# Optimization experiments

Measured on AMD Instinct MI355X. Metric: run time of the kernel, lower is better.

## Reference

```python
import jax, jax.numpy as jnp
import numpy as np

N, D_IN, FC_DIM, GROUP, NONGT, EMB = 4096, 12544, 1024, 16, 300, 64
DG = FC_DIM // GROUP  # 64 per-head dim


def extract_position_matrix(bbox, nongt_dim):
    xmin, ymin, xmax, ymax = jnp.split(bbox, 4, axis=1)  # each [N,1]
    bw = xmax - xmin + 1.0
    bh = ymax - ymin + 1.0
    cx = 0.5 * (xmin + xmax)
    cy = 0.5 * (ymin + ymax)
    dx = jnp.log(jnp.maximum(jnp.abs((cx - cx.T) / bw), 1e-3))
    dy = jnp.log(jnp.maximum(jnp.abs((cy - cy.T) / bh), 1e-3))
    dw = jnp.log(bw / bw.T)
    dh = jnp.log(bh / bh.T)
    # slice to first nongt_dim columns, stack -> [N, nongt, 4]
    return jnp.stack([dx[:, :nongt_dim], dy[:, :nongt_dim],
                      dw[:, :nongt_dim], dh[:, :nongt_dim]], axis=2)


def extract_position_embedding(pos_mat, feat_dim=64, wave_length=1000.0):
    n8 = feat_dim // 8
    feat_range = jnp.arange(n8, dtype=pos_mat.dtype)
    dim_mat = wave_length ** (8.0 / feat_dim * feat_range)  # [8]
    div = 100.0 * pos_mat[..., None] / dim_mat              # [N,nongt,4,8]
    emb = jnp.concatenate([jnp.sin(div), jnp.cos(div)], axis=3)  # [N,nongt,4,16]
    return emb.reshape(pos_mat.shape[0], pos_mat.shape[1], feat_dim)


def attention_multi_head(feat, pos_emb, Wpos, bpos, Wq, bq, Wk, bk, Wo, bo):
    # feat: [N, 1024], pos_emb: [N, nongt, 64]
    nongt_feat = feat[:NONGT]                                   # [nongt, 1024]
    aff_w = jax.nn.relu(pos_emb @ Wpos + bpos)                  # [N, nongt, G]
    aff_w = jnp.swapaxes(aff_w, 1, 2)                           # [N, G, nongt]
    q = (feat @ Wq + bq).reshape(-1, GROUP, DG)                 # [N, G, dg]
    k = (nongt_feat @ Wk + bk).reshape(NONGT, GROUP, DG)        # [nongt, G, dg]
    aff = jnp.einsum('ngd,mgd->ngm', q, k) * (1.0 / np.sqrt(DG))  # [N, G, nongt]
    logits = jnp.log(jnp.maximum(aff_w, 1e-6)) + aff
    p = jax.nn.softmax(logits, axis=2)                          # [N, G, nongt]
    out = jnp.einsum('ngm,mc->ngc', p, nongt_feat)              # [N, G, 1024]
    # grouped 1x1 conv: group g maps 1024 -> 64 outputs
    lin = jnp.einsum('ngc,goc->ngo', out, Wo) + bo.reshape(GROUP, DG)
    return lin.reshape(feat.shape[0], FC_DIM)


def setup_inputs() -> dict:
    key = jax.random.key(0)
    ks = jax.random.split(key, 20)
    roi_feat = jax.random.normal(ks[0], (N, D_IN), dtype=jnp.float32)
    u = jax.random.uniform(ks[1], (N, 4), dtype=jnp.float32)
    x1 = u[:, 0:1] * 500.0
    y1 = u[:, 1:2] * 500.0
    bbox = jnp.concatenate([x1, y1, x1 + u[:, 2:3] * 200.0 + 1.0,
                            y1 + u[:, 3:4] * 200.0 + 1.0], axis=1)
    def lin(k, fin, fout):
        s = 1.0 / np.sqrt(fin)
        return jax.random.normal(k, (fin, fout), dtype=jnp.float32) * s
    inp = {'roi_feat': roi_feat, 'bbox': bbox,
           'W_fc1': lin(ks[2], D_IN, FC_DIM), 'b_fc1': jnp.zeros((FC_DIM,), jnp.float32),
           'W_fc2': lin(ks[3], FC_DIM, FC_DIM), 'b_fc2': jnp.zeros((FC_DIM,), jnp.float32)}
    for i, base in [(1, 4), (2, 10)]:
        inp[f'Wpos{i}'] = lin(ks[base], EMB, GROUP)
        inp[f'bpos{i}'] = jnp.zeros((GROUP,), jnp.float32)
        inp[f'Wq{i}'] = lin(ks[base + 1], FC_DIM, FC_DIM)
        inp[f'bq{i}'] = jnp.zeros((FC_DIM,), jnp.float32)
        inp[f'Wk{i}'] = lin(ks[base + 2], FC_DIM, FC_DIM)
        inp[f'bk{i}'] = jnp.zeros((FC_DIM,), jnp.float32)
        inp[f'Wo{i}'] = jax.random.normal(ks[base + 3], (GROUP, DG, FC_DIM), dtype=jnp.float32) * (1.0 / np.sqrt(FC_DIM))
        inp[f'bo{i}'] = jnp.zeros((FC_DIM,), jnp.float32)
    return inp


def reference(roi_feat, bbox, W_fc1, b_fc1, W_fc2, b_fc2,
              Wpos1, bpos1, Wq1, bq1, Wk1, bk1, Wo1, bo1,
              Wpos2, bpos2, Wq2, bq2, Wk2, bk2, Wo2, bo2):
    pos_mat = extract_position_matrix(bbox, NONGT)
    pos_emb = extract_position_embedding(pos_mat, EMB)
    x = roi_feat
    for (Wf, bf, Wp, bp, Wq, bq, Wk, bk, Wo, bo) in [
        (W_fc1, b_fc1, Wpos1, bpos1, Wq1, bq1, Wk1, bk1, Wo1, bo1),
        (W_fc2, b_fc2, Wpos2, bpos2, Wq2, bq2, Wk2, bk2, Wo2, bo2)]:
        x = x @ Wf + bf
        attn = attention_multi_head(x, pos_emb, Wp, bp, Wq, bq, Wk, bk, Wo, bo)
        x = jax.nn.relu(x + attn)
    return x
```

## Files before the change

### kernel.cpp

```cpp
#include <hip/hip_runtime.h>


using bf16x8 = __attribute__((ext_vector_type(8))) short;
using f32x4  = __attribute__((ext_vector_type(4))) float;
typedef unsigned short u16;
typedef unsigned int   u32;

#define DEV __device__ __forceinline__

DEV u32 cvtpk(float lo, float hi) {
  u32 r;
  asm("v_cvt_pk_bf16_f32 %0, %1, %2" : "=v"(r) : "v"(lo), "v"(hi));
  return r;
}
DEV u16 f2bf(float f) { return (u16)cvtpk(f, f); }
DEV float bf2f(u16 h) { return __uint_as_float(((u32)h) << 16); }

DEV f32x4 mfma16(bf16x8 a, bf16x8 b, f32x4 c) {
  return __builtin_amdgcn_mfma_f32_16x16x32_bf16(a, b, c, 0, 0, 0);
}
DEV void gload16(const u16* g, u16* l) {
  __builtin_amdgcn_global_load_lds((const __attribute__((address_space(1))) void*)g,
                                   (__attribute__((address_space(3))) void*)l, 16, 0, 0);
}

DEV void fsincos(float x, float* s, float* c) {
  float r = x * 0.15915494309189535f;
  r -= rintf(r);
  float a = r * 6.283185307179586f;
  *s = __sinf(a); *c = __cosf(a);
}

__constant__ float C100D[8] = {100.f, 42.16965034285822f, 17.78279410038923f,
                               7.498942093324559f, 3.1622776601683795f,
                               1.333521432163324f, 0.5623413251903491f,
                               0.23713737056616552f};

struct PrepPosArgs {
  const float* bbox;
  const float* Wpos1; const float* Wpos2;
  const float* bpos1; const float* bpos2;
  u16* logw1; u16* logw2;
  const float* Wo1; u16* Wo1_b;
  const float* Wo2; u16* Wo2_b;
  const float* Wfc1; u16* Wfc1_t;
  const float* wsrc[5]; u16* wdst[5];
};

__global__ __launch_bounds__(256) void prep_pos_kernel(PrepPosArgs p) {
  __shared__ u16 pool[18944];
  int b = blockIdx.x, tid = threadIdx.x;
  if (b < 4096) {
    u16* emb_s = pool;
    u16* wp_s  = pool + 5632;
    u16* lw_s  = pool + 8448;
    int n = b;
    int w = tid >> 6, l = tid & 63, h = l >> 4, l15 = l & 15;
    for (int idx = tid; idx < 1024; idx += 256) {
      int e = idx >> 4, c = idx & 15;
      wp_s[c * 88 + e]        = f2bf(p.Wpos1[idx]);
      wp_s[(16 + c) * 88 + e] = f2bf(p.Wpos2[idx]);
    }
    float4 bn = ((const float4*)p.bbox)[n];
    float bw_n = bn.z - bn.x + 1.f, bh_n = bn.w - bn.y + 1.f;
    float cx_n = 0.5f * (bn.x + bn.z), cy_n = 0.5f * (bn.y + bn.w);
    float bps0 = p.bpos1[l15], bps1 = p.bpos2[l15];
    int pr = tid >> 2, k = tid & 3;

    for (int m0 = 0; m0 < 320; m0 += 64) {
      int m = m0 + pr;
      float4 bm = ((const float4*)p.bbox)[m];
      float v;
      if (k == 0)      v = logf(fmaxf(fabsf((cx_n - 0.5f * (bm.x + bm.z)) / bw_n), 1e-3f));
      else if (k == 1) v = logf(fmaxf(fabsf((cy_n - 0.5f * (bm.y + bm.w)) / bh_n), 1e-3f));
      else if (k == 2) v = logf(bw_n / (bm.z - bm.x + 1.f));
      else             v = logf(bh_n / (bm.w - bm.y + 1.f));
      __syncthreads();
#pragma unroll
      for (int tt = 0; tt < 8; tt++) {
        float s, c; fsincos(v * C100D[tt], &s, &c);
        emb_s[pr * 88 + k * 16 + tt]     = f2bf(s);
        emb_s[pr * 88 + k * 16 + 8 + tt] = f2bf(c);
      }
      __syncthreads();
      f32x4 acc0 = {0.f, 0.f, 0.f, 0.f}, acc1 = {0.f, 0.f, 0.f, 0.f};
      bf16x8 a0 = *(const bf16x8*)&emb_s[(w * 16 + l15) * 88 + h * 8];
      bf16x8 a1 = *(const bf16x8*)&emb_s[(w * 16 + l15) * 88 + 32 + h * 8];
      bf16x8 b00 = *(const bf16x8*)&wp_s[l15 * 88 + h * 8];
      bf16x8 b01 = *(const bf16x8*)&wp_s[l15 * 88 + 32 + h * 8];
      bf16x8 b10 = *(const bf16x8*)&wp_s[(16 + l15) * 88 + h * 8];
      bf16x8 b11 = *(const bf16x8*)&wp_s[(16 + l15) * 88 + 32 + h * 8];
      acc0 = mfma16(a0, b00, acc0); acc0 = mfma16(a1, b01, acc0);
      acc1 = mfma16(a0, b10, acc1); acc1 = mfma16(a1, b11, acc1);
#pragma unroll
      for (int r = 0; r < 4; r++) {
        int mm = m0 + w * 16 + h * 4 + r;
        lw_s[l15 * 328 + mm]        = f2bf(logf(fmaxf(acc0[r] + bps0, 1e-6f)));
        lw_s[(16 + l15) * 328 + mm] = f2bf(logf(fmaxf(acc1[r] + bps1, 1e-6f)));
      }
    }
    __syncthreads();
    for (int i = tid; i < 1280; i += 256) {
      int layer = i / 640, rest = i - layer * 640;
      int gg = rest / 40, seg = rest - gg * 40;
      bf16x8 v = *(const bf16x8*)&lw_s[(layer * 16 + gg) * 328 + seg * 8];
      u16* dst = (layer ? p.logw2 : p.logw1) + ((size_t)gg * 4096 + n) * 320 + seg * 8;
      *(bf16x8*)dst = v;
    }
    return;
  }
  int b2 = b - 4096;
  if (b2 < 1024) {
    const float* src = (b2 < 512) ? p.Wo1 : p.Wo2;
    u16* dst = (b2 < 512) ? p.Wo1_b : p.Wo2_b;
    size_t i = ((size_t)(b2 & 511) * 256 + tid) * 8;
    float4 a = *(const float4*)(src + i);
    float4 c = *(const float4*)(src + i + 4);
    int4 v;
    v.x = (int)cvtpk(a.x, a.y); v.y = (int)cvtpk(a.z, a.w);
    v.z = (int)cvtpk(c.x, c.y); v.w = (int)cvtpk(c.z, c.w);
    *(int4*)(dst + i) = v;
    return;
  }
  float (*tp)[36] = (float(*)[36])pool;
  const float* in; u16* out; int r0, c0, R, C;
  if (b2 < 13568) {
    int idx = b2 - 1024;
    in = p.Wfc1; out = p.Wfc1_t; R = 12544; C = 1024;
    r0 = (idx >> 5) * 32; c0 = (idx & 31) * 32;
  } else {
    int idx = b2 - 13568;
    int z = idx >> 10, rest = idx & 1023;
    in = p.wsrc[z]; out = p.wdst[z]; R = 1024; C = 1024;
    r0 = (rest >> 5) * 32; c0 = (rest & 31) * 32;
  }
  {
    int r = tid >> 3, c4 = (tid & 7) * 4;
    float4 v = *(const float4*)(in + (size_t)(r0 + r) * C + c0 + c4);
    *(float4*)&tp[r][c4] = v;
  }
  __syncthreads();
  {
    int c = tid >> 3, r4 = (tid & 7) * 4;
    int2 v;
    v.x = (int)cvtpk(tp[r4 + 0][c], tp[r4 + 1][c]);
    v.y = (int)cvtpk(tp[r4 + 2][c], tp[r4 + 3][c]);
    *(int2*)(out + (size_t)(c0 + c) * R + r0 + r4) = v;
  }
}

__global__ __launch_bounds__(512, 2) void gemm8p(
    const float* __restrict__ A, const u16* __restrict__ Bt,
    float* __restrict__ P) {
  const int K = 12544;
  __shared__ u16 lds[65536];
  int tid = threadIdx.x;
  int w = tid >> 6, l = tid & 63, h = l >> 4, l15 = l & 15;
  int wm = w >> 2, wn = w & 3;

  int b = ((blockIdx.x & 7) << 5) | (blockIdx.x >> 3);
  int bz = b >> 6, rest = b & 63;
  int bm = (rest & 15) * 256;
  int bn = (rest >> 4) * 256;
  size_t k0 = (size_t)bz * 3136;

  int arow = tid >> 3;
  int c0 = (tid & 7) * 8;
  const float* pA0 = A + (size_t)(bm + arow) * K + k0 + c0;
  const size_t aseg = (size_t)64 * K;
  int awe = ((arow * 128 + c0 * 2) ^ ((arow & 7) << 4)) >> 1;

  int X = ((tid >> 3) & 7) << 4;
  int lb2 = (tid * 16) ^ X;
  int lr = lb2 >> 7, lc = (lb2 & 127) >> 1;
  const u16* pB = Bt + (size_t)(bn + lr) * K + k0 + lc;
  const size_t o64 = (size_t)64 * K, o128 = (size_t)128 * K, o192 = (size_t)192 * K;

  int swz = (l15 & 7) << 3;
  int xk0 = (h * 8) ^ swz;
  int xk1 = 32 ^ xk0;
  int rA = (wm * 64 + l15) * 64;
  int rB = (wn * 32 + l15) * 64;

  f32x4 acc[8][4];
#pragma unroll
  for (int i = 0; i < 8; i++)
#pragma unroll
    for (int j = 0; j < 4; j++) acc[i][j] = (f32x4){0.f, 0.f, 0.f, 0.f};

  float4 a0[4], a1[4];
  bf16x8 af[4][2], bl[2][2], bh[2][2];

#define AISSUE(kk) { _Pragma("unroll") for (int s = 0; s < 4; s++) {     \
    a0[s] = *(const float4*)(pA0 + s * aseg + (kk));                     \
    a1[s] = *(const float4*)(pA0 + s * aseg + (kk) + 4); } }
#define BISSUE_LO(WB, kk) {                                              \
    gload16(pB + (kk),        (WB) + tid * 8);                           \
    gload16(pB + o64 + (kk),  (WB) + 4096 + tid * 8); }
#define BISSUE_HI(WB, kk) {                                              \
    gload16(pB + o128 + (kk), (WB) + 8192 + tid * 8);                    \
    gload16(pB + o192 + (kk), (WB) + 12288 + tid * 8); }
#define AWRITE(WA) { _Pragma("unroll") for (int s = 0; s < 4; s++) {     \
    int4 v;                                                              \
    v.x = (int)cvtpk(a0[s].x, a0[s].y);                                  \
    v.y = (int)cvtpk(a0[s].z, a0[s].w);                                  \
    v.z = (int)cvtpk(a1[s].x, a1[s].y);                                  \
    v.w = (int)cvtpk(a1[s].z, a1[s].w);                                  \
    *(int4*)&(WA)[awe + s * 4096] = v; } }
#define READ_AF(BASE)                                                    \
  _Pragma("unroll") for (int i = 0; i < 4; i++) {                        \
    af[i][0] = *(const bf16x8*)&LA[(BASE) + rA + i * 1024 + xk0];        \
    af[i][1] = *(const bf16x8*)&LA[(BASE) + rA + i * 1024 + xk1];        \
  }
#define READ_BL {                                                        \
  _Pragma("unroll") for (int j = 0; j < 2; j++) {                        \
    bl[j][0] = *(const bf16x8*)&LB[rB + j * 1024 + xk0];                 \
    bl[j][1] = *(const bf16x8*)&LB[rB + j * 1024 + xk1]; } }
#define READ_BH {                                                        \
  _Pragma("unroll") for (int j = 0; j < 2; j++) {                        \
    bh[j][0] = *(const bf16x8*)&LB[8192 + rB + j * 1024 + xk0];          \
    bh[j][1] = *(const bf16x8*)&LB[8192 + rB + j * 1024 + xk1]; } }
#define Q_MFMA(QR, QC, BF)                                               \
  __builtin_amdgcn_s_setprio(1);                                         \
  _Pragma("unroll") for (int i = 0; i < 4; i++)                          \
    _Pragma("unroll") for (int j = 0; j < 2; j++) {                      \
      acc[(QR)*4+i][(QC)*2+j] = mfma16(af[i][0], BF[j][0], acc[(QR)*4+i][(QC)*2+j]); \
      acc[(QR)*4+i][(QC)*2+j] = mfma16(af[i][1], BF[j][1], acc[(QR)*4+i][(QC)*2+j]); \
    }                                                                    \
  __builtin_amdgcn_s_setprio(0);
#define SBAR __builtin_amdgcn_sched_barrier(0)

  AISSUE(0);
  BISSUE_LO(lds + 16384, 0);
  BISSUE_HI(lds + 16384, 0);
  AWRITE(lds);
  asm volatile("s_waitcnt vmcnt(0) lgkmcnt(0)" ::: "memory");
  __builtin_amdgcn_s_barrier();

  for (int t = 0; t < 48; t++) {
    const u16* LA = lds + (t & 1) * 32768;
    const u16* LB = LA + 16384;
    u16* WA = lds + ((t + 1) & 1) * 32768;
    u16* WB = WA + 16384;
    int ktn = (t + 1) * 64;
    AISSUE(ktn);
    asm volatile("s_waitcnt vmcnt(10) lgkmcnt(0)" ::: "memory");
    __builtin_amdgcn_s_barrier();
    SBAR;
    READ_AF(0);
    READ_BL;
    Q_MFMA(0, 0, bl);
    SBAR;
    BISSUE_LO(WB, ktn);
    asm volatile("s_waitcnt vmcnt(10)" ::: "memory");
    __builtin_amdgcn_s_barrier();
    SBAR;
    READ_BH;
    Q_MFMA(0, 1, bh);
    SBAR;
    BISSUE_HI(WB, ktn);
    READ_AF(8192);
    Q_MFMA(1, 1, bh);
    SBAR;
    Q_MFMA(1, 0, bl);
    SBAR;
    AWRITE(WA);
  }
  {
    const u16* LA = lds;
    const u16* LB = lds + 16384;
    asm volatile("s_waitcnt vmcnt(2) lgkmcnt(0)" ::: "memory");
    __builtin_amdgcn_s_barrier();
    SBAR;
    READ_AF(0);
    READ_BL;
    Q_MFMA(0, 0, bl);
    SBAR;
    asm volatile("s_waitcnt vmcnt(0)" ::: "memory");
    __builtin_amdgcn_s_barrier();
    SBAR;
    READ_BH;
    Q_MFMA(0, 1, bh);
    SBAR;
    READ_AF(8192);
    Q_MFMA(1, 1, bh);
    Q_MFMA(1, 0, bl);
  }
#undef AISSUE
#undef BISSUE_LO
#undef BISSUE_HI
#undef AWRITE
#undef READ_AF
#undef READ_BL
#undef READ_BH
#undef Q_MFMA
#undef SBAR

  float* dst = P + (size_t)bz * 4096 * 1024;
#pragma unroll
  for (int qr = 0; qr < 2; qr++)
#pragma unroll
    for (int i = 0; i < 4; i++)
#pragma unroll
      for (int qc = 0; qc < 2; qc++)
#pragma unroll
        for (int j = 0; j < 2; j++) {
          int row0 = bm + qr * 128 + wm * 64 + i * 16 + h * 4;
          int col  = bn + qc * 128 + wn * 32 + j * 16 + l15;
          f32x4 v = acc[qr * 4 + i][qc * 2 + j];
#pragma unroll
          for (int r = 0; r < 4; r++)
            dst[(size_t)(row0 + r) * 1024 + col] = v[r];
        }
}

__global__ __launch_bounds__(256) void reduce_kernel(
    const float* __restrict__ P, const float* __restrict__ bias,
    u16* __restrict__ xb) {
  const size_t MN = (size_t)4096 * 1024;
  size_t i = ((size_t)blockIdx.x * 256 + threadIdx.x) * 4;
  size_t stride = (size_t)2048 * 256 * 4;
  for (; i < MN; i += stride) {
    float4 a = *(const float4*)(P + i);
    float4 b = *(const float4*)(P + MN + i);
    float4 c = *(const float4*)(P + 2 * MN + i);
    float4 d = *(const float4*)(P + 3 * MN + i);
    float4 bv = *(const float4*)(bias + (i & 1023));
    float4 r;
    r.x = a.x + b.x + c.x + d.x + bv.x;
    r.y = a.y + b.y + c.y + d.y + bv.y;
    r.z = a.z + b.z + c.z + d.z + bv.z;
    r.w = a.w + b.w + c.w + d.w + bv.w;
    int2 hv; hv.x = (int)cvtpk(r.x, r.y); hv.y = (int)cvtpk(r.z, r.w);
    *(int2*)(xb + i) = hv;
  }
}

struct GDesc {
  const u16* A; const u16* Bt; const float* bias;
  u16* Cb;
  int M, N, K, ldc, nt;
};

__global__ __launch_bounds__(256, 2) void gemmU(GDesc g0, GDesc g1, GDesc g2,
                                                int c0, int c1) {
  __shared__ u16 lds[32768];
  GDesc g; int lb = blockIdx.x;
  if (lb < c0) { g = g0; lb = (lb & 7) * (c0 >> 3) + (lb >> 3); }
  else if (lb < c1) { g = g1; lb -= c0; }
  else { g = g2; lb -= c1; }
  int bm = (lb / g.nt) * 128, bn = (lb % g.nt) * 128;
  int tid = threadIdx.x;
  int w = tid >> 6, l = tid & 63, h = l >> 4, l15 = l & 15;
  int wm = w >> 1, wn = w & 1;
  int K = g.K;

  int X = ((tid >> 3) & 7) << 4;
  int lbyte = (tid * 16) ^ X;
  int lr = lbyte >> 7, lc = (lbyte & 127) >> 1;
  const u16 *pa[4], *pb[4];
#pragma unroll
  for (int c = 0; c < 4; c++) {
    pa[c] = g.A  + (size_t)min(bm + c * 32 + lr, g.M - 1) * K + lc;
    pb[c] = g.Bt + (size_t)min(bn + c * 32 + lr, g.N - 1) * K + lc;
  }

  int swz = (l15 & 7) << 3;
  int xk0 = (h * 8) ^ swz;
  int xk1 = 32 ^ xk0;
  int rA = (wm * 64 + l15) * 64;
  int rB = (wn * 64 + l15) * 64;

  f32x4 acc[4][4];
#pragma unroll
  for (int i = 0; i < 4; i++)
#pragma unroll
    for (int j = 0; j < 4; j++) acc[i][j] = (f32x4){0.f, 0.f, 0.f, 0.f};

#define ISSUEU(W, kk)                                     \
  { gload16(pa[0] + (kk), (W) + tid * 8);                 \
    gload16(pa[1] + (kk), (W) + 2048 + tid * 8);          \
    gload16(pa[2] + (kk), (W) + 4096 + tid * 8);          \
    gload16(pa[3] + (kk), (W) + 6144 + tid * 8);          \
    gload16(pb[0] + (kk), (W) + 8192 + tid * 8);          \
    gload16(pb[1] + (kk), (W) + 10240 + tid * 8);         \
    gload16(pb[2] + (kk), (W) + 12288 + tid * 8);         \
    gload16(pb[3] + (kk), (W) + 14336 + tid * 8); }

  ISSUEU(lds, 0);
  int ktiles = K >> 6;
  for (int t = 0; t < ktiles; t++) {
    const u16* LA = lds + (t & 1) * 16384;
    const u16* LB = LA + 8192;
    u16* W = lds + ((t ^ 1) & 1) * 16384;
    if (t < ktiles - 1) {
      ISSUEU(W, (t + 1) * 64);
      asm volatile("s_waitcnt vmcnt(8)" ::: "memory");
    } else {
      asm volatile("s_waitcnt vmcnt(0)" ::: "memory");
    }
    __builtin_amdgcn_s_barrier();
    asm volatile("" ::: "memory");
    bf16x8 a[4][2], bfr[4][2];
#pragma unroll
    for (int i = 0; i < 4; i++) {
      a[i][0] = *(const bf16x8*)&LA[rA + i * 1024 + xk0];
      a[i][1] = *(const bf16x8*)&LA[rA + i * 1024 + xk1];
    }
#pragma unroll
    for (int j = 0; j < 4; j++) {
      bfr[j][0] = *(const bf16x8*)&LB[rB + j * 1024 + xk0];
      bfr[j][1] = *(const bf16x8*)&LB[rB + j * 1024 + xk1];
    }
    __builtin_amdgcn_s_setprio(1);
#pragma unroll
    for (int i = 0; i < 4; i++)
#pragma unroll
      for (int j = 0; j < 4; j++) {
        acc[i][j] = mfma16(a[i][0], bfr[j][0], acc[i][j]);
        acc[i][j] = mfma16(a[i][1], bfr[j][1], acc[i][j]);
      }
    __builtin_amdgcn_s_setprio(0);
    asm volatile("" ::: "memory");
    __builtin_amdgcn_s_barrier();
  }
#undef ISSUEU

#pragma unroll
  for (int i = 0; i < 4; i++) {
#pragma unroll
    for (int j = 0; j < 4; j++) {
      int col = bn + wn * 64 + j * 16 + l15;
      if (col >= g.ldc) continue;
      float bv = (g.bias != nullptr && col < g.N) ? g.bias[col] : 0.f;
      int row0 = bm + wm * 64 + i * 16 + h * 4;
#pragma unroll
      for (int r = 0; r < 4; r++) {
        int row = row0 + r;
        if (row >= g.M) continue;
        g.Cb[(size_t)row * g.ldc + col] = f2bf(acc[i][j][r] + bv);
      }
    }
  }
}

template <bool LAST>
__global__ __launch_bounds__(256) void attn_kernel(
    const u16* __restrict__ qb, const u16* __restrict__ kb,
    const u16* __restrict__ kvt, const u16* __restrict__ logw,
    const u16* __restrict__ xr, const float* __restrict__ bo,
    float* __restrict__ outf, u16* __restrict__ outb) {
  __shared__ u16 ps[64 * 344];
  int tid = threadIdx.x;
  int g = blockIdx.y, n0 = blockIdx.x * 64;
  int w = tid >> 6, l = tid & 63, h = l >> 4, l15 = l & 15;

  {
    const u16* src = logw + ((size_t)g * 4096 + n0) * 320;
    for (int i = tid; i < 64 * 40; i += 256) {
      int row = i / 40, seg = i - row * 40;
      *(bf16x8*)&ps[row * 328 + seg * 8] = *(const bf16x8*)(src + row * 320 + seg * 8);
    }
  }
  int nrow = n0 + w * 16 + l15;
  const u16* qp = qb + (size_t)nrow * 1024 + g * 64;
  bf16x8 aq0 = *(const bf16x8*)(qp + h * 8);
  bf16x8 aq1 = *(const bf16x8*)(qp + 32 + h * 8);

  f32x4 acc[19];
#pragma unroll
  for (int f = 0; f < 19; f++) acc[f] = (f32x4){0.f, 0.f, 0.f, 0.f};
  const u16* kp = kb + g * 64 + h * 8;
  __builtin_amdgcn_s_setprio(1);
#pragma unroll
  for (int f = 0; f < 19; f++) {
    bf16x8 b0 = *(const bf16x8*)(kp + (size_t)(f * 16 + l15) * 1024);
    bf16x8 b1 = *(const bf16x8*)(kp + (size_t)(f * 16 + l15) * 1024 + 32);
    acc[f] = mfma16(aq0, b0, acc[f]);
    acc[f] = mfma16(aq1, b1, acc[f]);
  }
  __builtin_amdgcn_s_setprio(0);
  __syncthreads();

  int nbase = n0 + w * 16 + h * 4;
  int lrow = w * 16 + h * 4;
  float mx[4] = {-INFINITY, -INFINITY, -INFINITY, -INFINITY};
  float sm[4] = {0.f, 0.f, 0.f, 0.f};
#pragma unroll
  for (int f = 0; f < 19; f++) {
    int m = f * 16 + l15;
#pragma unroll
    for (int r = 0; r < 4; r++) {
      float lw = -INFINITY;
      if (m < 300) lw = bf2f(ps[(lrow + r) * 328 + m]);
      float lg = acc[f][r] * 0.125f + lw;
      acc[f][r] = lg;
      mx[r] = fmaxf(mx[r], lg);
    }
  }
#pragma unroll
  for (int d = 1; d < 16; d <<= 1)
#pragma unroll
    for (int r = 0; r < 4; r++) mx[r] = fmaxf(mx[r], __shfl_xor(mx[r], d));
#pragma unroll
  for (int f = 0; f < 19; f++)
#pragma unroll
    for (int r = 0; r < 4; r++) {
      float p = __expf(acc[f][r] - mx[r]);
      acc[f][r] = p; sm[r] += p;
    }
#pragma unroll
  for (int d = 1; d < 16; d <<= 1)
#pragma unroll
    for (int r = 0; r < 4; r++) sm[r] += __shfl_xor(sm[r], d);
  float inv[4];
#pragma unroll
  for (int r = 0; r < 4; r++) inv[r] = 1.f / sm[r];

  __syncthreads();
#pragma unroll
  for (int f = 0; f < 19; f++)
#pragma unroll
    for (int r = 0; r < 4; r++)
      ps[(lrow + r) * 344 + f * 16 + l15] = f2bf(acc[f][r]);
#pragma unroll
  for (int r = 0; r < 4; r++)
    ps[(lrow + r) * 344 + 304 + l15] = 0;

  f32x4 acc2[4];
#pragma unroll
  for (int fo = 0; fo < 4; fo++) acc2[fo] = (f32x4){0.f, 0.f, 0.f, 0.f};
  const u16* vp = kvt + (size_t)g * 64 * 320 + h * 8;
  __builtin_amdgcn_s_setprio(1);
#pragma unroll
  for (int ks = 0; ks < 10; ks++) {
    bf16x8 ap = *(const bf16x8*)&ps[(w * 16 + l15) * 344 + ks * 32 + h * 8];
#pragma unroll
    for (int fo = 0; fo < 4; fo++) {
      bf16x8 bv = *(const bf16x8*)(vp + (size_t)(fo * 16 + l15) * 320 + ks * 32);
      acc2[fo] = mfma16(ap, bv, acc2[fo]);
    }
  }
  __builtin_amdgcn_s_setprio(0);
#pragma unroll
  for (int fo = 0; fo < 4; fo++) {
    int col = g * 64 + fo * 16 + l15;
    float bov = bo[col];
#pragma unroll
    for (int r = 0; r < 4; r++) {
      int row = nbase + r;
      size_t off = (size_t)row * 1024 + col;
      float v = bf2f(xr[off]) + acc2[fo][r] * inv[r] + bov;
      v = fmaxf(v, 0.f);
      if (LAST) outf[off] = v;
      else      outb[off] = f2bf(v);
    }
  }
}

extern "C" void kernel_launch(void* const* d_in, const int* in_sizes, int n_in,
                              void* d_out, int out_size, void* d_ws, size_t ws_size,
                              hipStream_t stream) {
  (void)in_sizes; (void)n_in; (void)out_size; (void)ws_size;
  const float* roi   = (const float*)d_in[0];
  const float* bbox  = (const float*)d_in[1];
  const float* Wfc1  = (const float*)d_in[2];
  const float* bfc1  = (const float*)d_in[3];
  const float* Wfc2  = (const float*)d_in[4];
  const float* bfc2  = (const float*)d_in[5];
  const float* Wpos1 = (const float*)d_in[6];
  const float* bpos1 = (const float*)d_in[7];
  const float* Wq1   = (const float*)d_in[8];
  const float* bq1   = (const float*)d_in[9];
  const float* Wk1   = (const float*)d_in[10];
  const float* bk1   = (const float*)d_in[11];
  const float* Wo1   = (const float*)d_in[12];
  const float* bo1   = (const float*)d_in[13];
  const float* Wpos2 = (const float*)d_in[14];
  const float* bpos2 = (const float*)d_in[15];
  const float* Wq2   = (const float*)d_in[16];
  const float* bq2   = (const float*)d_in[17];
  const float* Wk2   = (const float*)d_in[18];
  const float* bk2   = (const float*)d_in[19];
  const float* Wo2   = (const float*)d_in[20];
  const float* bo2   = (const float*)d_in[21];

  char* ws = (char*)d_ws;
  u16*  Wfc1_t = (u16*)(ws + 102760448);
  u16*  Wfc2_t = (u16*)(ws + 128450560);
  u16*  Wq1_t  = (u16*)(ws + 130547712);
  u16*  Wk1_t  = (u16*)(ws + 132644864);
  u16*  Wq2_t  = (u16*)(ws + 134742016);
  u16*  Wk2_t  = (u16*)(ws + 136839168);
  u16*  Wo1_b  = (u16*)(ws + 138936320);
  u16*  Wo2_b  = (u16*)(ws + 141033472);
  float* Pp    = (float*)(ws + 143134720);
  u16*  xb_f   = (u16*)(ws + 243798016);
  u16*  xb_a   = (u16*)(ws + 252186624);
  u16*  q_b    = (u16*)(ws + 260575232);
  u16*  k_b    = (u16*)(ws + 268963840);
  u16*  kvt_b  = (u16*)(ws + 269578240);
  u16*  logw1  = (u16*)(ws + 270233600);
  u16*  logw2  = (u16*)(ws + 312176640);

  {
    PrepPosArgs p;
    p.bbox = bbox;
    p.Wpos1 = Wpos1; p.Wpos2 = Wpos2;
    p.bpos1 = bpos1; p.bpos2 = bpos2;
    p.logw1 = logw1; p.logw2 = logw2;
    p.Wo1 = Wo1;   p.Wo1_b = Wo1_b;
    p.Wo2 = Wo2;   p.Wo2_b = Wo2_b;
    p.Wfc1 = Wfc1; p.Wfc1_t = Wfc1_t;
    p.wsrc[0] = Wfc2; p.wdst[0] = Wfc2_t;
    p.wsrc[1] = Wq1;  p.wdst[1] = Wq1_t;
    p.wsrc[2] = Wk1;  p.wdst[2] = Wk1_t;
    p.wsrc[3] = Wq2;  p.wdst[3] = Wq2_t;
    p.wsrc[4] = Wk2;  p.wdst[4] = Wk2_t;
    prep_pos_kernel<<<22784, 256, 0, stream>>>(p);
  }
  gemm8p<<<256, 512, 0, stream>>>(roi, Wfc1_t, Pp);
  reduce_kernel<<<2048, 256, 0, stream>>>(Pp, bfc1, xb_f);
  {
    GDesc q  = {xb_f,  Wq1_t, bq1, q_b,   4096, 1024, 1024, 1024, 8};
    GDesc kk = {xb_f,  Wk1_t, bk1, k_b,    300, 1024, 1024, 1024, 8};
    GDesc kv = {Wo1_b, xb_f,  nullptr, kvt_b, 1024, 300, 1024, 320, 3};
    gemmU<<<304, 256, 0, stream>>>(q, kk, kv, 256, 280);
  }
  attn_kernel<false><<<dim3(64, 16), 256, 0, stream>>>(q_b, k_b, kvt_b, logw1, xb_f, bo1, nullptr, xb_a);

  {
    GDesc fc = {xb_a, Wfc2_t, bfc2, xb_f, 4096, 1024, 1024, 1024, 8};
    gemmU<<<256, 256, 0, stream>>>(fc, fc, fc, 256, 256);
  }
  {
    GDesc q  = {xb_f,  Wq2_t, bq2, q_b,   4096, 1024, 1024, 1024, 8};
    GDesc kk = {xb_f,  Wk2_t, bk2, k_b,    300, 1024, 1024, 1024, 8};
    GDesc kv = {Wo2_b, xb_f,  nullptr, kvt_b, 1024, 300, 1024, 320, 3};
    gemmU<<<304, 256, 0, stream>>>(q, kk, kv, 256, 280);
  }
  attn_kernel<true><<<dim3(64, 16), 256, 0, stream>>>(q_b, k_b, kvt_b, logw2, xb_f, bo2, (float*)d_out, nullptr);
}
```

Before: 405.4 us.

## Move position/weight prep out of critical path, merge with split-K reduce

The prep kernel now only transposes Wfc1, so the big fc1 GEMM can start sooner. The position-embedding log-weights, the Wo bf16 casts and the small weight transposes move into a combined kernel with the split-K reduce that runs after the GEMM. The intent is to shorten the chain ahead of the GEMM and pack the memory-bound reduce together with the compute-heavy position work. Separately, s_setprio hints are removed from the attention kernel's MFMA loops.

```diff
diff --git a/kernel.cpp b/kernel.cpp
--- a/kernel.cpp
+++ b/kernel.cpp
@@ -36,107 +36,15 @@
                                1.333521432163324f, 0.5623413251903491f,
                                0.23713737056616552f};
 
-struct PrepPosArgs {
-  const float* bbox;
-  const float* Wpos1; const float* Wpos2;
-  const float* bpos1; const float* bpos2;
-  u16* logw1; u16* logw2;
-  const float* Wo1; u16* Wo1_b;
-  const float* Wo2; u16* Wo2_b;
-  const float* Wfc1; u16* Wfc1_t;
-  const float* wsrc[5]; u16* wdst[5];
-};
-
-__global__ __launch_bounds__(256) void prep_pos_kernel(PrepPosArgs p) {
-  __shared__ u16 pool[18944];
+__global__ __launch_bounds__(256) void prep_kernel(const float* __restrict__ Wfc1,
+                                                   u16* __restrict__ Wfc1_t) {
+  __shared__ float tp[32][36];
   int b = blockIdx.x, tid = threadIdx.x;
-  if (b < 4096) {
-    u16* emb_s = pool;
-    u16* wp_s  = pool + 5632;
-    u16* lw_s  = pool + 8448;
-    int n = b;
-    int w = tid >> 6, l = tid & 63, h = l >> 4, l15 = l & 15;
-    for (int idx = tid; idx < 1024; idx += 256) {
-      int e = idx >> 4, c = idx & 15;
-      wp_s[c * 88 + e]        = f2bf(p.Wpos1[idx]);
-      wp_s[(16 + c) * 88 + e] = f2bf(p.Wpos2[idx]);
-    }
-    float4 bn = ((const float4*)p.bbox)[n];
-    float bw_n = bn.z - bn.x + 1.f, bh_n = bn.w - bn.y + 1.f;
-    float cx_n = 0.5f * (bn.x + bn.z), cy_n = 0.5f * (bn.y + bn.w);
-    float bps0 = p.bpos1[l15], bps1 = p.bpos2[l15];
-    int pr = tid >> 2, k = tid & 3;
-
-    for (int m0 = 0; m0 < 320; m0 += 64) {
-      int m = m0 + pr;
-      float4 bm = ((const float4*)p.bbox)[m];
-      float v;
-      if (k == 0)      v = logf(fmaxf(fabsf((cx_n - 0.5f * (bm.x + bm.z)) / bw_n), 1e-3f));
-      else if (k == 1) v = logf(fmaxf(fabsf((cy_n - 0.5f * (bm.y + bm.w)) / bh_n), 1e-3f));
-      else if (k == 2) v = logf(bw_n / (bm.z - bm.x + 1.f));
-      else             v = logf(bh_n / (bm.w - bm.y + 1.f));
-      __syncthreads();
-#pragma unroll
-      for (int tt = 0; tt < 8; tt++) {
-        float s, c; fsincos(v * C100D[tt], &s, &c);
-        emb_s[pr * 88 + k * 16 + tt]     = f2bf(s);
-        emb_s[pr * 88 + k * 16 + 8 + tt] = f2bf(c);
-      }
-      __syncthreads();
-      f32x4 acc0 = {0.f, 0.f, 0.f, 0.f}, acc1 = {0.f, 0.f, 0.f, 0.f};
-      bf16x8 a0 = *(const bf16x8*)&emb_s[(w * 16 + l15) * 88 + h * 8];
-      bf16x8 a1 = *(const bf16x8*)&emb_s[(w * 16 + l15) * 88 + 32 + h * 8];
-      bf16x8 b00 = *(const bf16x8*)&wp_s[l15 * 88 + h * 8];
-      bf16x8 b01 = *(const bf16x8*)&wp_s[l15 * 88 + 32 + h * 8];
-      bf16x8 b10 = *(const bf16x8*)&wp_s[(16 + l15) * 88 + h * 8];
-      bf16x8 b11 = *(const bf16x8*)&wp_s[(16 + l15) * 88 + 32 + h * 8];
-      acc0 = mfma16(a0, b00, acc0); acc0 = mfma16(a1, b01, acc0);
-      acc1 = mfma16(a0, b10, acc1); acc1 = mfma16(a1, b11, acc1);
-#pragma unroll
-      for (int r = 0; r < 4; r++) {
-        int mm = m0 + w * 16 + h * 4 + r;
-        lw_s[l15 * 328 + mm]        = f2bf(logf(fmaxf(acc0[r] + bps0, 1e-6f)));
-        lw_s[(16 + l15) * 328 + mm] = f2bf(logf(fmaxf(acc1[r] + bps1, 1e-6f)));
-      }
-    }
-    __syncthreads();
-    for (int i = tid; i < 1280; i += 256) {
-      int layer = i / 640, rest = i - layer * 640;
-      int gg = rest / 40, seg = rest - gg * 40;
-      bf16x8 v = *(const bf16x8*)&lw_s[(layer * 16 + gg) * 328 + seg * 8];
-      u16* dst = (layer ? p.logw2 : p.logw1) + ((size_t)gg * 4096 + n) * 320 + seg * 8;
-      *(bf16x8*)dst = v;
-    }
-    return;
-  }
-  int b2 = b - 4096;
-  if (b2 < 1024) {
-    const float* src = (b2 < 512) ? p.Wo1 : p.Wo2;
-    u16* dst = (b2 < 512) ? p.Wo1_b : p.Wo2_b;
-    size_t i = ((size_t)(b2 & 511) * 256 + tid) * 8;
-    float4 a = *(const float4*)(src + i);
-    float4 c = *(const float4*)(src + i + 4);
-    int4 v;
-    v.x = (int)cvtpk(a.x, a.y); v.y = (int)cvtpk(a.z, a.w);
-    v.z = (int)cvtpk(c.x, c.y); v.w = (int)cvtpk(c.z, c.w);
-    *(int4*)(dst + i) = v;
-    return;
-  }
-  float (*tp)[36] = (float(*)[36])pool;
-  const float* in; u16* out; int r0, c0, R, C;
-  if (b2 < 13568) {
-    int idx = b2 - 1024;
-    in = p.Wfc1; out = p.Wfc1_t; R = 12544; C = 1024;
-    r0 = (idx >> 5) * 32; c0 = (idx & 31) * 32;
-  } else {
-    int idx = b2 - 13568;
-    int z = idx >> 10, rest = idx & 1023;
-    in = p.wsrc[z]; out = p.wdst[z]; R = 1024; C = 1024;
-    r0 = (rest >> 5) * 32; c0 = (rest & 31) * 32;
-  }
+  const int R = 12544, C = 1024;
+  int r0 = (b >> 5) * 32, c0 = (b & 31) * 32;
   {
     int r = tid >> 3, c4 = (tid & 7) * 4;
-    float4 v = *(const float4*)(in + (size_t)(r0 + r) * C + c0 + c4);
+    float4 v = *(const float4*)(Wfc1 + (size_t)(r0 + r) * C + c0 + c4);
     *(float4*)&tp[r][c4] = v;
   }
   __syncthreads();
@@ -145,7 +53,7 @@
     int2 v;
     v.x = (int)cvtpk(tp[r4 + 0][c], tp[r4 + 1][c]);
     v.y = (int)cvtpk(tp[r4 + 2][c], tp[r4 + 3][c]);
-    *(int2*)(out + (size_t)(c0 + c) * R + r0 + r4) = v;
+    *(int2*)(Wfc1_t + (size_t)(c0 + c) * R + r0 + r4) = v;
   }
 }
 
@@ -314,25 +222,132 @@
         }
 }
 
-__global__ __launch_bounds__(256) void reduce_kernel(
-    const float* __restrict__ P, const float* __restrict__ bias,
-    u16* __restrict__ xb) {
-  const size_t MN = (size_t)4096 * 1024;
-  size_t i = ((size_t)blockIdx.x * 256 + threadIdx.x) * 4;
-  size_t stride = (size_t)2048 * 256 * 4;
-  for (; i < MN; i += stride) {
-    float4 a = *(const float4*)(P + i);
-    float4 b = *(const float4*)(P + MN + i);
-    float4 c = *(const float4*)(P + 2 * MN + i);
-    float4 d = *(const float4*)(P + 3 * MN + i);
-    float4 bv = *(const float4*)(bias + (i & 1023));
-    float4 r;
-    r.x = a.x + b.x + c.x + d.x + bv.x;
-    r.y = a.y + b.y + c.y + d.y + bv.y;
-    r.z = a.z + b.z + c.z + d.z + bv.z;
-    r.w = a.w + b.w + c.w + d.w + bv.w;
-    int2 hv; hv.x = (int)cvtpk(r.x, r.y); hv.y = (int)cvtpk(r.z, r.w);
-    *(int2*)(xb + i) = hv;
+struct RPArgs {
+  const float* P; const float* bias; u16* xb;
+  const float* bbox;
+  const float* Wpos1; const float* Wpos2;
+  const float* bpos1; const float* bpos2;
+  u16* logw1; u16* logw2;
+  const float* Wo1; u16* Wo1_b;
+  const float* Wo2; u16* Wo2_b;
+  const float* wsrc[5]; u16* wdst[5];
+};
+
+__global__ __launch_bounds__(256) void reduce_pos_kernel(RPArgs p) {
+  __shared__ u16 pool[18944];
+  int tid = threadIdx.x;
+  int b = blockIdx.x;
+  if (b < 2048) {
+    const size_t MN = (size_t)4096 * 1024;
+    size_t i = ((size_t)b * 256 + tid) * 4;
+    size_t stride = (size_t)2048 * 256 * 4;
+    for (; i < MN; i += stride) {
+      float4 a = *(const float4*)(p.P + i);
+      float4 b2 = *(const float4*)(p.P + MN + i);
+      float4 c = *(const float4*)(p.P + 2 * MN + i);
+      float4 d = *(const float4*)(p.P + 3 * MN + i);
+      float4 bv = *(const float4*)(p.bias + (i & 1023));
+      float4 r;
+      r.x = a.x + b2.x + c.x + d.x + bv.x;
+      r.y = a.y + b2.y + c.y + d.y + bv.y;
+      r.z = a.z + b2.z + c.z + d.z + bv.z;
+      r.w = a.w + b2.w + c.w + d.w + bv.w;
+      int2 hv; hv.x = (int)cvtpk(r.x, r.y); hv.y = (int)cvtpk(r.z, r.w);
+      *(int2*)(p.xb + i) = hv;
+    }
+    return;
+  }
+  if (b < 6144) {
+    u16* emb_s = pool;
+    u16* wp_s  = pool + 5632;
+    u16* lw_s  = pool + 8448;
+    int n = b - 2048;
+    int w = tid >> 6, l = tid & 63, h = l >> 4, l15 = l & 15;
+    for (int idx = tid; idx < 1024; idx += 256) {
+      int e = idx >> 4, c = idx & 15;
+      wp_s[c * 88 + e]        = f2bf(p.Wpos1[idx]);
+      wp_s[(16 + c) * 88 + e] = f2bf(p.Wpos2[idx]);
+    }
+    float4 bn = ((const float4*)p.bbox)[n];
+    float bw_n = bn.z - bn.x + 1.f, bh_n = bn.w - bn.y + 1.f;
+    float cx_n = 0.5f * (bn.x + bn.z), cy_n = 0.5f * (bn.y + bn.w);
+    float bps0 = p.bpos1[l15], bps1 = p.bpos2[l15];
+    int pr = tid >> 2, k = tid & 3;
+
+    for (int m0 = 0; m0 < 320; m0 += 64) {
+      int m = m0 + pr;
+      float4 bm = ((const float4*)p.bbox)[m];
+      float v;
+      if (k == 0)      v = logf(fmaxf(fabsf((cx_n - 0.5f * (bm.x + bm.z)) / bw_n), 1e-3f));
+      else if (k == 1) v = logf(fmaxf(fabsf((cy_n - 0.5f * (bm.y + bm.w)) / bh_n), 1e-3f));
+      else if (k == 2) v = logf(bw_n / (bm.z - bm.x + 1.f));
+      else             v = logf(bh_n / (bm.w - bm.y + 1.f));
+      __syncthreads();
+#pragma unroll
+      for (int tt = 0; tt < 8; tt++) {
+        float s, c; fsincos(v * C100D[tt], &s, &c);
+        emb_s[pr * 88 + k * 16 + tt]     = f2bf(s);
+        emb_s[pr * 88 + k * 16 + 8 + tt] = f2bf(c);
+      }
+      __syncthreads();
+      f32x4 acc0 = {0.f, 0.f, 0.f, 0.f}, acc1 = {0.f, 0.f, 0.f, 0.f};
+      bf16x8 a0 = *(const bf16x8*)&emb_s[(w * 16 + l15) * 88 + h * 8];
+      bf16x8 a1 = *(const bf16x8*)&emb_s[(w * 16 + l15) * 88 + 32 + h * 8];
+      bf16x8 b00 = *(const bf16x8*)&wp_s[l15 * 88 + h * 8];
+      bf16x8 b01 = *(const bf16x8*)&wp_s[l15 * 88 + 32 + h * 8];
+      bf16x8 b10 = *(const bf16x8*)&wp_s[(16 + l15) * 88 + h * 8];
+      bf16x8 b11 = *(const bf16x8*)&wp_s[(16 + l15) * 88 + 32 + h * 8];
+      acc0 = mfma16(a0, b00, acc0); acc0 = mfma16(a1, b01, acc0);
+      acc1 = mfma16(a0, b10, acc1); acc1 = mfma16(a1, b11, acc1);
+#pragma unroll
+      for (int r = 0; r < 4; r++) {
+        int mm = m0 + w * 16 + h * 4 + r;
+        lw_s[l15 * 328 + mm]        = f2bf(logf(fmaxf(acc0[r] + bps0, 1e-6f)));
+        lw_s[(16 + l15) * 328 + mm] = f2bf(logf(fmaxf(acc1[r] + bps1, 1e-6f)));
+      }
+    }
+    __syncthreads();
+    for (int i = tid; i < 1280; i += 256) {
+      int layer = i / 640, rest = i - layer * 640;
+      int gg = rest / 40, seg = rest - gg * 40;
+      bf16x8 v = *(const bf16x8*)&lw_s[(layer * 16 + gg) * 328 + seg * 8];
+      u16* dst = (layer ? p.logw2 : p.logw1) + ((size_t)gg * 4096 + n) * 320 + seg * 8;
+      *(bf16x8*)dst = v;
+    }
+    return;
+  }
+  if (b < 7168) {
+    int b2 = b - 6144;
+    const float* src = (b2 < 512) ? p.Wo1 : p.Wo2;
+    u16* dst = (b2 < 512) ? p.Wo1_b : p.Wo2_b;
+    size_t i = ((size_t)(b2 & 511) * 256 + tid) * 8;
+    float4 a = *(const float4*)(src + i);
+    float4 c = *(const float4*)(src + i + 4);
+    int4 v;
+    v.x = (int)cvtpk(a.x, a.y); v.y = (int)cvtpk(a.z, a.w);
+    v.z = (int)cvtpk(c.x, c.y); v.w = (int)cvtpk(c.z, c.w);
+    *(int4*)(dst + i) = v;
+    return;
+  }
+  {
+    float (*tp)[36] = (float(*)[36])pool;
+    int idx = b - 7168;
+    int z = idx >> 10, rest = idx & 1023;
+    const float* in = p.wsrc[z]; u16* out = p.wdst[z];
+    int r0 = (rest >> 5) * 32, c0 = (rest & 31) * 32;
+    {
+      int r = tid >> 3, c4 = (tid & 7) * 4;
+      float4 v = *(const float4*)(in + (size_t)(r0 + r) * 1024 + c0 + c4);
+      *(float4*)&tp[r][c4] = v;
+    }
+    __syncthreads();
+    {
+      int c = tid >> 3, r4 = (tid & 7) * 4;
+      int2 v;
+      v.x = (int)cvtpk(tp[r4 + 0][c], tp[r4 + 1][c]);
+      v.y = (int)cvtpk(tp[r4 + 2][c], tp[r4 + 3][c]);
+      *(int2*)(out + (size_t)(c0 + c) * 1024 + r0 + r4) = v;
+    }
   }
 }
 
@@ -471,7 +486,6 @@
 #pragma unroll
   for (int f = 0; f < 19; f++) acc[f] = (f32x4){0.f, 0.f, 0.f, 0.f};
   const u16* kp = kb + g * 64 + h * 8;
-  __builtin_amdgcn_s_setprio(1);
 #pragma unroll
   for (int f = 0; f < 19; f++) {
     bf16x8 b0 = *(const bf16x8*)(kp + (size_t)(f * 16 + l15) * 1024);
@@ -479,7 +493,6 @@
     acc[f] = mfma16(aq0, b0, acc[f]);
     acc[f] = mfma16(aq1, b1, acc[f]);
   }
-  __builtin_amdgcn_s_setprio(0);
   __syncthreads();
 
   int nbase = n0 + w * 16 + h * 4;
@@ -531,7 +544,6 @@
 #pragma unroll
   for (int fo = 0; fo < 4; fo++) acc2[fo] = (f32x4){0.f, 0.f, 0.f, 0.f};
   const u16* vp = kvt + (size_t)g * 64 * 320 + h * 8;
-  __builtin_amdgcn_s_setprio(1);
 #pragma unroll
   for (int ks = 0; ks < 10; ks++) {
     bf16x8 ap = *(const bf16x8*)&ps[(w * 16 + l15) * 344 + ks * 32 + h * 8];
@@ -541,7 +553,6 @@
       acc2[fo] = mfma16(ap, bv, acc2[fo]);
     }
   }
-  __builtin_amdgcn_s_setprio(0);
 #pragma unroll
   for (int fo = 0; fo < 4; fo++) {
     int col = g * 64 + fo * 16 + l15;
@@ -603,24 +614,24 @@
   u16*  logw1  = (u16*)(ws + 270233600);
   u16*  logw2  = (u16*)(ws + 312176640);
 
-  {
-    PrepPosArgs p;
+  prep_kernel<<<12544, 256, 0, stream>>>(Wfc1, Wfc1_t);
+  gemm8p<<<256, 512, 0, stream>>>(roi, Wfc1_t, Pp);
+  {
+    RPArgs p;
+    p.P = Pp; p.bias = bfc1; p.xb = xb_f;
     p.bbox = bbox;
     p.Wpos1 = Wpos1; p.Wpos2 = Wpos2;
     p.bpos1 = bpos1; p.bpos2 = bpos2;
     p.logw1 = logw1; p.logw2 = logw2;
-    p.Wo1 = Wo1;   p.Wo1_b = Wo1_b;
-    p.Wo2 = Wo2;   p.Wo2_b = Wo2_b;
-    p.Wfc1 = Wfc1; p.Wfc1_t = Wfc1_t;
+    p.Wo1 = Wo1; p.Wo1_b = Wo1_b;
+    p.Wo2 = Wo2; p.Wo2_b = Wo2_b;
     p.wsrc[0] = Wfc2; p.wdst[0] = Wfc2_t;
     p.wsrc[1] = Wq1;  p.wdst[1] = Wq1_t;
     p.wsrc[2] = Wk1;  p.wdst[2] = Wk1_t;
     p.wsrc[3] = Wq2;  p.wdst[3] = Wq2_t;
     p.wsrc[4] = Wk2;  p.wdst[4] = Wk2_t;
-    prep_pos_kernel<<<22784, 256, 0, stream>>>(p);
-  }
-  gemm8p<<<256, 512, 0, stream>>>(roi, Wfc1_t, Pp);
-  reduce_kernel<<<2048, 256, 0, stream>>>(Pp, bfc1, xb_f);
+    reduce_pos_kernel<<<12288, 256, 0, stream>>>(p);
+  }
   {
     GDesc q  = {xb_f,  Wq1_t, bq1, q_b,   4096, 1024, 1024, 1024, 8};
     GDesc kk = {xb_f,  Wk1_t, bk1, k_b,    300, 1024, 1024, 1024, 8};
```

New measurement: 377.1 us. 1.07x faster.
